# Performance work log

Measured on AMD Instinct MI355X. Metric: run time of the kernel, lower is better.

## Reference

```python
import jax, jax.numpy as jnp
import numpy as np

N = 50000          # nodes
E = 625000         # edges
H = 128            # hidden_dim
L = 4              # num_layers
G = 2000           # number of graphs in batch
NODE_F = 9
EDGE_F = 4
LN_EPS = 1e-5


def setup_inputs() -> dict:
    key = jax.random.key(0)
    ks = jax.random.split(key, 14)
    s = 0.05
    return {
        "x": jax.random.normal(ks[0], (N, NODE_F), jnp.float32),
        "edge_index": jax.random.randint(ks[1], (2, E), 0, N, dtype=jnp.int32),
        "edge_attr": jax.random.normal(ks[2], (E, EDGE_F), jnp.float32),
        "batch": jnp.sort(jax.random.randint(ks[3], (N,), 0, G, dtype=jnp.int32)),
        # node / edge encoders
        "Wn": jax.random.normal(ks[4], (NODE_F, H), jnp.float32) * s,
        "bn": jnp.zeros((H,), jnp.float32),
        "We": jax.random.normal(ks[5], (EDGE_F, H), jnp.float32) * s,
        "be": jnp.zeros((H,), jnp.float32),
        # per-layer GINE MLP params (stacked over layers)
        "W1": jax.random.normal(ks[6], (L, H, 2 * H), jnp.float32) * s,
        "b1": jnp.zeros((L, 2 * H), jnp.float32),
        "W2": jax.random.normal(ks[7], (L, 2 * H, H), jnp.float32) * s,
        "b2": jnp.zeros((L, H), jnp.float32),
        # per-layer LayerNorm params
        "gamma": jnp.ones((L, H), jnp.float32),
        "beta": jnp.zeros((L, H), jnp.float32),
    }


def reference(x, edge_index, edge_attr, batch, Wn, bn, We, be, W1, b1, W2, b2, gamma, beta):
    h = x @ Wn + bn                       # [N, H]
    ea = edge_attr @ We + be              # [E, H]
    src, dst = edge_index[0], edge_index[1]
    for l in range(L):
        res = h
        # GINEConv (eps=0): out = mlp(x + sum_j relu(x_j + e_ij))
        msg = jax.nn.relu(h[src] + ea)                              # [E, H] gather+add+relu
        agg = jax.ops.segment_sum(msg, dst, num_segments=N)        # scatter-sum -> [N, H]
        z = h + agg
        z = jax.nn.relu(z @ W1[l] + b1[l]) @ W2[l] + b2[l]          # 2-layer MLP
        mu = jnp.mean(z, axis=-1, keepdims=True)
        var = jnp.mean((z - mu) ** 2, axis=-1, keepdims=True)
        z = (z - mu) * jax.lax.rsqrt(var + LN_EPS) * gamma[l] + beta[l]
        h = jax.nn.relu(z) + res                                    # relu + residual
    # global_add_pool
    return jax.ops.segment_sum(h, batch, num_segments=G)            # [G, H]
```

## Files before the change

### kernel.cpp

```cpp
#include <hip/hip_runtime.h>

typedef unsigned short ushort_t;
typedef __attribute__((ext_vector_type(8))) __bf16 bf16x8;
typedef __attribute__((ext_vector_type(4))) float f32x4;

#define HD 128
#define NL 4
#define SCAN_C 2048

__device__ __forceinline__ ushort_t f2bf(float f){
  unsigned u = __builtin_bit_cast(unsigned, f);
  unsigned r = (u + 0x7FFFu + ((u >> 16) & 1u)) >> 16;
  return (ushort_t)r;
}

__device__ __forceinline__ float bf2f(ushort_t u){
  unsigned v = ((unsigned)u) << 16;
  return __builtin_bit_cast(float, v);
}

__device__ __forceinline__ f32x4 mfma16(bf16x8 a, bf16x8 b, f32x4 c){
  return __builtin_amdgcn_mfma_f32_16x16x32_bf16(a, b, c, 0, 0, 0);
}

__global__ void hist_kernel(const int* __restrict__ dst, int* __restrict__ deg, int E){
  int e = blockIdx.x * 256 + threadIdx.x;
  if (e < E) atomicAdd(&deg[dst[e]], 1);
}

__global__ void gbound_kernel(const int* __restrict__ batch, int* __restrict__ goff,
                              int N, int G){
  int n = blockIdx.x * 256 + threadIdx.x;
  if (n >= N) return;
  int bc = batch[n];
  int bp = (n == 0) ? -1 : batch[n - 1];
  for (int g = bp + 1; g <= bc; ++g) goff[g] = n;
  if (n == N - 1)
    for (int g = bc + 1; g <= G; ++g) goff[g] = N;
}

__global__ void scan_part(const int* __restrict__ in, int* __restrict__ bsum, int n){
  int b = blockIdx.x, tid = threadIdx.x;
  int base = b * SCAN_C + tid * 8;
  int s = 0;
  if (base + 8 <= n){
    int4 a = *(const int4*)(in + base);
    int4 c = *(const int4*)(in + base + 4);
    s = a.x + a.y + a.z + a.w + c.x + c.y + c.z + c.w;
  } else {
    #pragma unroll
    for (int k = 0; k < 8; ++k) if (base + k < n) s += in[base + k];
  }
  #pragma unroll
  for (int o = 1; o < 64; o <<= 1) s += __shfl_xor(s, o, 64);
  __shared__ int ws[4];
  int lane = tid & 63, wid = tid >> 6;
  if (lane == 0) ws[wid] = s;
  __syncthreads();
  if (tid == 0) bsum[b] = ws[0] + ws[1] + ws[2] + ws[3];
}

__global__ void scan_top(const int* __restrict__ bsum, int* __restrict__ bofs,
                         int* __restrict__ outn, int B){
  int tid = threadIdx.x;
  int v = (tid < B) ? bsum[tid] : 0;
  int lane = tid & 63, wid = tid >> 6;
  int inc = v;
  #pragma unroll
  for (int o = 1; o < 64; o <<= 1){
    int t = __shfl_up(inc, o, 64);
    if (lane >= o) inc += t;
  }
  __shared__ int ws[4];
  if (lane == 63) ws[wid] = inc;
  __syncthreads();
  int wprev = 0;
  for (int i = 0; i < wid; ++i) wprev += ws[i];
  if (tid < B) bofs[tid] = inc - v + wprev;
  if (tid == 0) *outn = ws[0] + ws[1] + ws[2] + ws[3];
}

__global__ void scan_final(const int* __restrict__ in, const int* __restrict__ bofs,
                           int* __restrict__ out, int* __restrict__ cur, int n){
  int b = blockIdx.x, tid = threadIdx.x;
  int base = b * SCAN_C + tid * 8;
  int v[8];
  if (base + 8 <= n){
    *(int4*)(v)     = *(const int4*)(in + base);
    *(int4*)(v + 4) = *(const int4*)(in + base + 4);
  } else {
    #pragma unroll
    for (int k = 0; k < 8; ++k) v[k] = (base + k < n) ? in[base + k] : 0;
  }
  int tsum = 0;
  #pragma unroll
  for (int k = 0; k < 8; ++k) tsum += v[k];
  int lane = tid & 63, wid = tid >> 6;
  int inc = tsum;
  #pragma unroll
  for (int o = 1; o < 64; o <<= 1){
    int t = __shfl_up(inc, o, 64);
    if (lane >= o) inc += t;
  }
  __shared__ int ws[4];
  if (lane == 63) ws[wid] = inc;
  __syncthreads();
  int run = bofs[b] + inc - tsum;
  for (int i = 0; i < wid; ++i) run += ws[i];
  #pragma unroll
  for (int k = 0; k < 8; ++k){
    int i = base + k;
    if (i < n){
      out[i] = run;
      if (cur) cur[i] = run;
      run += v[k];
    }
  }
}

__global__ void scatter_kernel(const int* __restrict__ dst, int* __restrict__ cursor,
                               int* __restrict__ perm, int E){
  int e = blockIdx.x * 256 + threadIdx.x;
  if (e < E){
    int d = dst[e];
    int p = atomicAdd(&cursor[d], 1);
    perm[p] = e;
  }
}

__global__ void permute_kernel(const int* __restrict__ perm, const int* __restrict__ src,
                               const float4* __restrict__ ea, int* __restrict__ srcs_s,
                               float4* __restrict__ ea4p, int E){
  int p = blockIdx.x * 256 + threadIdx.x;
  if (p < E){
    int e = perm[p];
    srcs_s[p] = src[e];
    ea4p[p] = ea[e];
  }
}

__global__ void wconv_kernel(const float* __restrict__ W1, const float* __restrict__ W2,
                             ushort_t* __restrict__ W1t, ushort_t* __restrict__ W2t){
  int i = blockIdx.x * 256 + threadIdx.x;
  if (i < NL * 32768){
    int l = i >> 15, r = i & 32767;
    int n = r >> 7, k = r & 127;
    W1t[i] = f2bf(W1[l * 32768 + k * 256 + n]);
  } else {
    int i2 = i - NL * 32768;
    int l = i2 >> 15, r = i2 & 32767;
    int n = r >> 8, k = r & 255;
    W2t[i2] = f2bf(W2[l * 32768 + k * 128 + n]);
  }
}

__global__ void encoder_kernel(const float* __restrict__ x, const float* __restrict__ Wn,
                               const float* __restrict__ bn, float* __restrict__ h,
                               ushort_t* __restrict__ hb, int N){
  int n = blockIdx.x, j = threadIdx.x;
  float acc = bn[j];
  #pragma unroll
  for (int k = 0; k < 9; ++k) acc = fmaf(x[n * 9 + k], Wn[k * HD + j], acc);
  h[(size_t)n * HD + j] = acc;
  hb[(size_t)n * HD + j] = f2bf(acc);
}

__global__ void agg_kernel(const float* __restrict__ h, const ushort_t* __restrict__ hb,
                           const int* __restrict__ off, const int* __restrict__ srcs,
                           const float4* __restrict__ ea4, const float* __restrict__ We,
                           const float* __restrict__ be, ushort_t* __restrict__ z, int N){
  int n = blockIdx.x, j = threadIdx.x;
  float w0 = We[j], w1 = We[HD + j], w2 = We[2 * HD + j], w3 = We[3 * HD + j];
  float bj = be[j];
  int s = off[n], e = off[n + 1];
  float acc = h[(size_t)n * HD + j];
  int i = s;
  for (; i + 8 <= e; i += 8){
    int s0 = srcs[i],     s1 = srcs[i + 1], s2 = srcs[i + 2], s3 = srcs[i + 3];
    int s4 = srcs[i + 4], s5 = srcs[i + 5], s6 = srcs[i + 6], s7 = srcs[i + 7];
    ushort_t g0 = hb[(size_t)s0 * HD + j];
    ushort_t g1 = hb[(size_t)s1 * HD + j];
    ushort_t g2 = hb[(size_t)s2 * HD + j];
    ushort_t g3 = hb[(size_t)s3 * HD + j];
    ushort_t g4 = hb[(size_t)s4 * HD + j];
    ushort_t g5 = hb[(size_t)s5 * HD + j];
    ushort_t g6 = hb[(size_t)s6 * HD + j];
    ushort_t g7 = hb[(size_t)s7 * HD + j];
    {
      float4 a0 = ea4[i], a1 = ea4[i + 1], a2 = ea4[i + 2], a3 = ea4[i + 3];
      float e0 = fmaf(a0.x, w0, fmaf(a0.y, w1, fmaf(a0.z, w2, fmaf(a0.w, w3, bj))));
      float e1 = fmaf(a1.x, w0, fmaf(a1.y, w1, fmaf(a1.z, w2, fmaf(a1.w, w3, bj))));
      float e2 = fmaf(a2.x, w0, fmaf(a2.y, w1, fmaf(a2.z, w2, fmaf(a2.w, w3, bj))));
      float e3 = fmaf(a3.x, w0, fmaf(a3.y, w1, fmaf(a3.z, w2, fmaf(a3.w, w3, bj))));
      acc += fmaxf(bf2f(g0) + e0, 0.f);
      acc += fmaxf(bf2f(g1) + e1, 0.f);
      acc += fmaxf(bf2f(g2) + e2, 0.f);
      acc += fmaxf(bf2f(g3) + e3, 0.f);
    }
    {
      float4 a4 = ea4[i + 4], a5 = ea4[i + 5], a6 = ea4[i + 6], a7 = ea4[i + 7];
      float e4 = fmaf(a4.x, w0, fmaf(a4.y, w1, fmaf(a4.z, w2, fmaf(a4.w, w3, bj))));
      float e5 = fmaf(a5.x, w0, fmaf(a5.y, w1, fmaf(a5.z, w2, fmaf(a5.w, w3, bj))));
      float e6 = fmaf(a6.x, w0, fmaf(a6.y, w1, fmaf(a6.z, w2, fmaf(a6.w, w3, bj))));
      float e7 = fmaf(a7.x, w0, fmaf(a7.y, w1, fmaf(a7.z, w2, fmaf(a7.w, w3, bj))));
      acc += fmaxf(bf2f(g4) + e4, 0.f);
      acc += fmaxf(bf2f(g5) + e5, 0.f);
      acc += fmaxf(bf2f(g6) + e6, 0.f);
      acc += fmaxf(bf2f(g7) + e7, 0.f);
    }
  }
  for (; i + 4 <= e; i += 4){
    int s0 = srcs[i], s1 = srcs[i + 1], s2 = srcs[i + 2], s3 = srcs[i + 3];
    float4 a0 = ea4[i], a1 = ea4[i + 1], a2 = ea4[i + 2], a3 = ea4[i + 3];
    float h0 = bf2f(hb[(size_t)s0 * HD + j]);
    float h1 = bf2f(hb[(size_t)s1 * HD + j]);
    float h2 = bf2f(hb[(size_t)s2 * HD + j]);
    float h3 = bf2f(hb[(size_t)s3 * HD + j]);
    float e0 = fmaf(a0.x, w0, fmaf(a0.y, w1, fmaf(a0.z, w2, fmaf(a0.w, w3, bj))));
    float e1 = fmaf(a1.x, w0, fmaf(a1.y, w1, fmaf(a1.z, w2, fmaf(a1.w, w3, bj))));
    float e2 = fmaf(a2.x, w0, fmaf(a2.y, w1, fmaf(a2.z, w2, fmaf(a2.w, w3, bj))));
    float e3 = fmaf(a3.x, w0, fmaf(a3.y, w1, fmaf(a3.z, w2, fmaf(a3.w, w3, bj))));
    acc += fmaxf(h0 + e0, 0.f);
    acc += fmaxf(h1 + e1, 0.f);
    acc += fmaxf(h2 + e2, 0.f);
    acc += fmaxf(h3 + e3, 0.f);
  }
  for (; i < e; ++i){
    int sc = srcs[i];
    float4 a = ea4[i];
    float eav = fmaf(a.x, w0, fmaf(a.y, w1, fmaf(a.z, w2, fmaf(a.w, w3, bj))));
    acc += fmaxf(bf2f(hb[(size_t)sc * HD + j]) + eav, 0.f);
  }
  z[(size_t)n * HD + j] = f2bf(acc);
}

__global__ __launch_bounds__(512, 4) void mlp_fused_kernel(
    const ushort_t* __restrict__ zin, const ushort_t* __restrict__ W1t,
    const float* __restrict__ b1, const ushort_t* __restrict__ W2t,
    const float* __restrict__ b2, const float* __restrict__ gamma,
    const float* __restrict__ beta, float* __restrict__ h,
    ushort_t* __restrict__ hb, int N){
  extern __shared__ char lds[];
  int tid = threadIdx.x;
  int r0 = blockIdx.x * 128;
  #pragma unroll
  for (int i = 0; i < 4; ++i){
    int g = i * 512 + tid;
    int row = g >> 4, kg = g & 15;
    int lb = row * 256 + ((kg * 16) ^ ((row & 7) << 4));
    int ar = min(r0 + row, N - 1);
    *(bf16x8*)(lds + lb) = *(const bf16x8*)(zin + (size_t)ar * 128 + kg * 8);
  }
  int w = tid >> 6, l = tid & 63;
  int lr = l & 15, lk = l >> 4;
  int wk = w >> 1, wn = w & 1;
  bf16x8 aN[4];
  #pragma unroll
  for (int fm = 0; fm < 4; ++fm)
    aN[fm] = *(const bf16x8*)((const char*)W1t +
              (size_t)(wk * 64 + fm * 16 + lr) * 256 + lk * 16);
  __syncthreads();
  {
    f32x4 acc1[4][4] = {};
    #pragma unroll
    for (int ks = 0; ks < 4; ++ks){
      int kb = ks * 64 + lk * 16;
      bf16x8 aC[4];
      #pragma unroll
      for (int fm = 0; fm < 4; ++fm) aC[fm] = aN[fm];
      if (ks < 3){
        int kbn = (ks + 1) * 64 + lk * 16;
        #pragma unroll
        for (int fm = 0; fm < 4; ++fm)
          aN[fm] = *(const bf16x8*)((const char*)W1t +
                    (size_t)(wk * 64 + fm * 16 + lr) * 256 + kbn);
      }
      bf16x8 b[4];
      #pragma unroll
      for (int fn = 0; fn < 4; ++fn){
        int node = wn * 64 + fn * 16 + lr;
        b[fn] = *(const bf16x8*)(lds + node * 256 + (kb ^ ((node & 7) << 4)));
      }
      #pragma unroll
      for (int fm = 0; fm < 4; ++fm)
        #pragma unroll
        for (int fn = 0; fn < 4; ++fn)
          acc1[fm][fn] = mfma16(aC[fm], b[fn], acc1[fm][fn]);
    }
    __syncthreads();
    #pragma unroll
    for (int fm = 0; fm < 4; ++fm){
      f32x4 bv = *(const f32x4*)(b1 + wk * 64 + fm * 16 + lk * 4);
      int k2b = (wk * 64 + fm * 16 + lk * 4) * 2;
      #pragma unroll
      for (int fn = 0; fn < 4; ++fn){
        int node = wn * 64 + fn * 16 + lr;
        ushort4 tv;
        tv.x = f2bf(fmaxf(acc1[fm][fn][0] + bv[0], 0.f));
        tv.y = f2bf(fmaxf(acc1[fm][fn][1] + bv[1], 0.f));
        tv.z = f2bf(fmaxf(acc1[fm][fn][2] + bv[2], 0.f));
        tv.w = f2bf(fmaxf(acc1[fm][fn][3] + bv[3], 0.f));
        *(ushort4*)(lds + node * 512 + (k2b ^ ((node & 7) << 4))) = tv;
      }
    }
  }
  int wd = w >> 1, wn2 = w & 1;
  bf16x8 a2N[2];
  #pragma unroll
  for (int fm = 0; fm < 2; ++fm)
    a2N[fm] = *(const bf16x8*)((const char*)W2t +
               (size_t)(wd * 32 + fm * 16 + lr) * 512 + lk * 16);
  __syncthreads();
  f32x4 acc2[2][4] = {};
  #pragma unroll
  for (int ks = 0; ks < 8; ++ks){
    int kb = ks * 64 + lk * 16;
    bf16x8 a2C[2];
    #pragma unroll
    for (int fm = 0; fm < 2; ++fm) a2C[fm] = a2N[fm];
    if (ks < 7){
      int kbn = (ks + 1) * 64 + lk * 16;
      #pragma unroll
      for (int fm = 0; fm < 2; ++fm)
        a2N[fm] = *(const bf16x8*)((const char*)W2t +
                   (size_t)(wd * 32 + fm * 16 + lr) * 512 + kbn);
    }
    bf16x8 bt2[4];
    #pragma unroll
    for (int fn = 0; fn < 4; ++fn){
      int node = wn2 * 64 + fn * 16 + lr;
      bt2[fn] = *(const bf16x8*)(lds + node * 512 + (kb ^ ((node & 7) << 4)));
    }
    #pragma unroll
    for (int fm = 0; fm < 2; ++fm)
      #pragma unroll
      for (int fn = 0; fn < 4; ++fn)
        acc2[fm][fn] = mfma16(a2C[fm], bt2[fn], acc2[fm][fn]);
  }
  __syncthreads();
  float* stat_s = (float*)lds;
  float* stat_q = (float*)(lds + 2048);
  f32x4 b2v[2], gv[2], btv[2];
  #pragma unroll
  for (int fm = 0; fm < 2; ++fm){
    int db = wd * 32 + fm * 16 + lk * 4;
    b2v[fm] = *(const f32x4*)(b2 + db);
    gv[fm]  = *(const f32x4*)(gamma + db);
    btv[fm] = *(const f32x4*)(beta + db);
  }
  #pragma unroll
  for (int fn = 0; fn < 4; ++fn){
    float ss = 0.f, qq = 0.f;
    #pragma unroll
    for (int fm = 0; fm < 2; ++fm)
      #pragma unroll
      for (int r = 0; r < 4; ++r){
        float v = acc2[fm][fn][r] + b2v[fm][r];
        acc2[fm][fn][r] = v;
        ss += v; qq += v * v;
      }
    ss += __shfl_xor(ss, 16, 64); ss += __shfl_xor(ss, 32, 64);
    qq += __shfl_xor(qq, 16, 64); qq += __shfl_xor(qq, 32, 64);
    if (l < 16){
      int node = wn2 * 64 + fn * 16 + lr;
      stat_s[node * 4 + wd] = ss;
      stat_q[node * 4 + wd] = qq;
    }
  }
  __syncthreads();
  #pragma unroll
  for (int fn = 0; fn < 4; ++fn){
    int node = wn2 * 64 + fn * 16 + lr;
    int gn = r0 + node;
    float ss = stat_s[node * 4 + 0] + stat_s[node * 4 + 1] +
               stat_s[node * 4 + 2] + stat_s[node * 4 + 3];
    float qq = stat_q[node * 4 + 0] + stat_q[node * 4 + 1] +
               stat_q[node * 4 + 2] + stat_q[node * 4 + 3];
    float mean = ss * (1.f / 128.f);
    float rs = rsqrtf(qq * (1.f / 128.f) - mean * mean + 1e-5f);
    if (gn < N){
      #pragma unroll
      for (int fm = 0; fm < 2; ++fm){
        int db = wd * 32 + fm * 16 + lk * 4;
        f32x4 hold = *(const f32x4*)(h + (size_t)gn * HD + db);
        f32x4 ov;
        #pragma unroll
        for (int r = 0; r < 4; ++r)
          ov[r] = fmaxf((acc2[fm][fn][r] - mean) * rs * gv[fm][r] + btv[fm][r], 0.f) + hold[r];
        *(f32x4*)(h + (size_t)gn * HD + db) = ov;
        ushort4 hv;
        hv.x = f2bf(ov[0]); hv.y = f2bf(ov[1]); hv.z = f2bf(ov[2]); hv.w = f2bf(ov[3]);
        *(ushort4*)(hb + (size_t)gn * HD + db) = hv;
      }
    }
  }
}

__global__ void pool_kernel(const float* __restrict__ h, const int* __restrict__ goff,
                            float* __restrict__ outp, int G){
  int g = blockIdx.x, j = threadIdx.x;
  int s = goff[g], e = goff[g + 1];
  float acc = 0.f;
  for (int i = s; i < e; ++i) acc += h[(size_t)i * HD + j];
  outp[(size_t)g * HD + j] = acc;
}

extern "C" void kernel_launch(void* const* d_in, const int* in_sizes, int n_in,
                              void* d_out, int out_size, void* d_ws, size_t ws_size,
                              hipStream_t stream){
  const float* x     = (const float*)d_in[0];
  const int*   ei    = (const int*)  d_in[1];
  const float* eattr = (const float*)d_in[2];
  const int*   batch = (const int*)  d_in[3];
  const float* Wn    = (const float*)d_in[4];
  const float* bn    = (const float*)d_in[5];
  const float* We    = (const float*)d_in[6];
  const float* be    = (const float*)d_in[7];
  const float* W1    = (const float*)d_in[8];
  const float* b1    = (const float*)d_in[9];
  const float* W2    = (const float*)d_in[10];
  const float* b2    = (const float*)d_in[11];
  const float* gamma = (const float*)d_in[12];
  const float* beta  = (const float*)d_in[13];
  float* outp = (float*)d_out;

  int N = in_sizes[3];
  int E = in_sizes[2] / 4;
  int G = out_size / HD;

  char* base = (char*)d_ws;
  size_t o = 0;
  auto alloc = [&](size_t bytes)->char*{
    char* r = base + o; o = (o + bytes + 255) & ~(size_t)255; return r;
  };
  float*    h    = (float*)   alloc((size_t)N * HD * 4);
  ushort_t* hb   = (ushort_t*)alloc((size_t)N * HD * 2);
  ushort_t* z    = (ushort_t*)alloc((size_t)N * HD * 2);
  ushort_t* W1t  = (ushort_t*)alloc((size_t)NL * 2 * HD * HD * 2);
  ushort_t* W2t  = (ushort_t*)alloc((size_t)NL * 2 * HD * HD * 2);
  int* deg    = (int*)alloc((size_t)N * 4);
  int* off    = (int*)alloc((size_t)(N + 1) * 4);
  int* goff   = (int*)alloc((size_t)(G + 1) * 4);
  int* cursor = (int*)alloc((size_t)N * 4);
  int* bsumN  = (int*)alloc(512 * 4);
  int* bofsN  = (int*)alloc(512 * 4);
  int* perm   = (int*)alloc((size_t)E * 4);
  int* srcs_s = (int*)alloc((size_t)E * 4);
  float4* ea4p= (float4*)alloc((size_t)E * 16);
  (void)ws_size; (void)n_in;

  const int* src = ei;
  const int* dst = ei + E;

  hipMemsetAsync(deg, 0, (size_t)N * 4, stream);

  hist_kernel<<<(E + 255) / 256, 256, 0, stream>>>(dst, deg, E);
  gbound_kernel<<<(N + 255) / 256, 256, 0, stream>>>(batch, goff, N, G);

  int BN = (N + SCAN_C - 1) / SCAN_C;
  scan_part<<<BN, 256, 0, stream>>>(deg, bsumN, N);
  scan_top<<<1, 256, 0, stream>>>(bsumN, bofsN, off + N, BN);
  scan_final<<<BN, 256, 0, stream>>>(deg, bofsN, off, cursor, N);

  scatter_kernel<<<(E + 255) / 256, 256, 0, stream>>>(dst, cursor, perm, E);
  permute_kernel<<<(E + 255) / 256, 256, 0, stream>>>(perm, src, (const float4*)eattr,
                                                      srcs_s, ea4p, E);
  wconv_kernel<<<(2 * NL * 32768) / 256, 256, 0, stream>>>(W1, W2, W1t, W2t);
  encoder_kernel<<<N, HD, 0, stream>>>(x, Wn, bn, h, hb, N);

  int mblocks = (N + 127) / 128;
  for (int l = 0; l < NL; ++l){
    agg_kernel<<<N, HD, 0, stream>>>(h, hb, off, srcs_s, ea4p, We, be, z, N);
    mlp_fused_kernel<<<mblocks, 512, 65536, stream>>>(
        z, W1t + (size_t)l * 2 * HD * HD, b1 + l * 2 * HD,
        W2t + (size_t)l * 2 * HD * HD, b2 + l * HD,
        gamma + l * HD, beta + l * HD, h, hb, N);
  }
  pool_kernel<<<G, HD, 0, stream>>>(h, goff, outp, G);
}
```

Baseline: 404.0 us.

## Fuse neighbor aggregation into the MLP layer kernel with ping-pong bf16 buffers

```diff
diff --git a/kernel.cpp b/kernel.cpp
--- a/kernel.cpp
+++ b/kernel.cpp
@@ -165,91 +165,90 @@
   hb[(size_t)n * HD + j] = f2bf(acc);
 }
 
-__global__ void agg_kernel(const float* __restrict__ h, const ushort_t* __restrict__ hb,
-                           const int* __restrict__ off, const int* __restrict__ srcs,
-                           const float4* __restrict__ ea4, const float* __restrict__ We,
-                           const float* __restrict__ be, ushort_t* __restrict__ z, int N){
-  int n = blockIdx.x, j = threadIdx.x;
-  float w0 = We[j], w1 = We[HD + j], w2 = We[2 * HD + j], w3 = We[3 * HD + j];
-  float bj = be[j];
-  int s = off[n], e = off[n + 1];
-  float acc = h[(size_t)n * HD + j];
-  int i = s;
-  for (; i + 8 <= e; i += 8){
-    int s0 = srcs[i],     s1 = srcs[i + 1], s2 = srcs[i + 2], s3 = srcs[i + 3];
-    int s4 = srcs[i + 4], s5 = srcs[i + 5], s6 = srcs[i + 6], s7 = srcs[i + 7];
-    ushort_t g0 = hb[(size_t)s0 * HD + j];
-    ushort_t g1 = hb[(size_t)s1 * HD + j];
-    ushort_t g2 = hb[(size_t)s2 * HD + j];
-    ushort_t g3 = hb[(size_t)s3 * HD + j];
-    ushort_t g4 = hb[(size_t)s4 * HD + j];
-    ushort_t g5 = hb[(size_t)s5 * HD + j];
-    ushort_t g6 = hb[(size_t)s6 * HD + j];
-    ushort_t g7 = hb[(size_t)s7 * HD + j];
-    {
-      float4 a0 = ea4[i], a1 = ea4[i + 1], a2 = ea4[i + 2], a3 = ea4[i + 3];
-      float e0 = fmaf(a0.x, w0, fmaf(a0.y, w1, fmaf(a0.z, w2, fmaf(a0.w, w3, bj))));
-      float e1 = fmaf(a1.x, w0, fmaf(a1.y, w1, fmaf(a1.z, w2, fmaf(a1.w, w3, bj))));
-      float e2 = fmaf(a2.x, w0, fmaf(a2.y, w1, fmaf(a2.z, w2, fmaf(a2.w, w3, bj))));
-      float e3 = fmaf(a3.x, w0, fmaf(a3.y, w1, fmaf(a3.z, w2, fmaf(a3.w, w3, bj))));
-      acc += fmaxf(bf2f(g0) + e0, 0.f);
-      acc += fmaxf(bf2f(g1) + e1, 0.f);
-      acc += fmaxf(bf2f(g2) + e2, 0.f);
-      acc += fmaxf(bf2f(g3) + e3, 0.f);
-    }
-    {
-      float4 a4 = ea4[i + 4], a5 = ea4[i + 5], a6 = ea4[i + 6], a7 = ea4[i + 7];
-      float e4 = fmaf(a4.x, w0, fmaf(a4.y, w1, fmaf(a4.z, w2, fmaf(a4.w, w3, bj))));
-      float e5 = fmaf(a5.x, w0, fmaf(a5.y, w1, fmaf(a5.z, w2, fmaf(a5.w, w3, bj))));
-      float e6 = fmaf(a6.x, w0, fmaf(a6.y, w1, fmaf(a6.z, w2, fmaf(a6.w, w3, bj))));
-      float e7 = fmaf(a7.x, w0, fmaf(a7.y, w1, fmaf(a7.z, w2, fmaf(a7.w, w3, bj))));
-      acc += fmaxf(bf2f(g4) + e4, 0.f);
-      acc += fmaxf(bf2f(g5) + e5, 0.f);
-      acc += fmaxf(bf2f(g6) + e6, 0.f);
-      acc += fmaxf(bf2f(g7) + e7, 0.f);
-    }
-  }
-  for (; i + 4 <= e; i += 4){
-    int s0 = srcs[i], s1 = srcs[i + 1], s2 = srcs[i + 2], s3 = srcs[i + 3];
-    float4 a0 = ea4[i], a1 = ea4[i + 1], a2 = ea4[i + 2], a3 = ea4[i + 3];
-    float h0 = bf2f(hb[(size_t)s0 * HD + j]);
-    float h1 = bf2f(hb[(size_t)s1 * HD + j]);
-    float h2 = bf2f(hb[(size_t)s2 * HD + j]);
-    float h3 = bf2f(hb[(size_t)s3 * HD + j]);
-    float e0 = fmaf(a0.x, w0, fmaf(a0.y, w1, fmaf(a0.z, w2, fmaf(a0.w, w3, bj))));
-    float e1 = fmaf(a1.x, w0, fmaf(a1.y, w1, fmaf(a1.z, w2, fmaf(a1.w, w3, bj))));
-    float e2 = fmaf(a2.x, w0, fmaf(a2.y, w1, fmaf(a2.z, w2, fmaf(a2.w, w3, bj))));
-    float e3 = fmaf(a3.x, w0, fmaf(a3.y, w1, fmaf(a3.z, w2, fmaf(a3.w, w3, bj))));
-    acc += fmaxf(h0 + e0, 0.f);
-    acc += fmaxf(h1 + e1, 0.f);
-    acc += fmaxf(h2 + e2, 0.f);
-    acc += fmaxf(h3 + e3, 0.f);
-  }
-  for (; i < e; ++i){
-    int sc = srcs[i];
-    float4 a = ea4[i];
-    float eav = fmaf(a.x, w0, fmaf(a.y, w1, fmaf(a.z, w2, fmaf(a.w, w3, bj))));
-    acc += fmaxf(bf2f(hb[(size_t)sc * HD + j]) + eav, 0.f);
-  }
-  z[(size_t)n * HD + j] = f2bf(acc);
-}
-
-__global__ __launch_bounds__(512, 4) void mlp_fused_kernel(
-    const ushort_t* __restrict__ zin, const ushort_t* __restrict__ W1t,
-    const float* __restrict__ b1, const ushort_t* __restrict__ W2t,
-    const float* __restrict__ b2, const float* __restrict__ gamma,
-    const float* __restrict__ beta, float* __restrict__ h,
-    ushort_t* __restrict__ hb, int N){
+__global__ __launch_bounds__(512, 4) void layer_kernel(
+    float* __restrict__ h, const ushort_t* __restrict__ hbi,
+    ushort_t* __restrict__ hbo, const int* __restrict__ off,
+    const int* __restrict__ srcs, const float4* __restrict__ ea4,
+    const float* __restrict__ We, const float* __restrict__ be,
+    const ushort_t* __restrict__ W1t, const float* __restrict__ b1,
+    const ushort_t* __restrict__ W2t, const float* __restrict__ b2,
+    const float* __restrict__ gamma, const float* __restrict__ beta, int N){
   extern __shared__ char lds[];
   int tid = threadIdx.x;
   int r0 = blockIdx.x * 128;
-  #pragma unroll
-  for (int i = 0; i < 4; ++i){
-    int g = i * 512 + tid;
-    int row = g >> 4, kg = g & 15;
-    int lb = row * 256 + ((kg * 16) ^ ((row & 7) << 4));
-    int ar = min(r0 + row, N - 1);
-    *(bf16x8*)(lds + lb) = *(const bf16x8*)(zin + (size_t)ar * 128 + kg * 8);
+  {
+    int j = tid & 127;
+    int q = tid >> 7;
+    float w0 = We[j], w1 = We[HD + j], w2 = We[2 * HD + j], w3 = We[3 * HD + j];
+    float bj = be[j];
+    for (int c = 0; c < 32; ++c){
+      int nl = q * 32 + c;
+      int node = r0 + nl;
+      float acc = 0.f;
+      if (node < N){
+        int s = off[node], e = off[node + 1];
+        acc = h[(size_t)node * HD + j];
+        int i = s;
+        for (; i + 8 <= e; i += 8){
+          int s0 = srcs[i],     s1 = srcs[i + 1], s2 = srcs[i + 2], s3 = srcs[i + 3];
+          int s4 = srcs[i + 4], s5 = srcs[i + 5], s6 = srcs[i + 6], s7 = srcs[i + 7];
+          ushort_t g0 = hbi[(size_t)s0 * HD + j];
+          ushort_t g1 = hbi[(size_t)s1 * HD + j];
+          ushort_t g2 = hbi[(size_t)s2 * HD + j];
+          ushort_t g3 = hbi[(size_t)s3 * HD + j];
+          ushort_t g4 = hbi[(size_t)s4 * HD + j];
+          ushort_t g5 = hbi[(size_t)s5 * HD + j];
+          ushort_t g6 = hbi[(size_t)s6 * HD + j];
+          ushort_t g7 = hbi[(size_t)s7 * HD + j];
+          {
+            float4 a0 = ea4[i], a1 = ea4[i + 1], a2 = ea4[i + 2], a3 = ea4[i + 3];
+            float e0 = fmaf(a0.x, w0, fmaf(a0.y, w1, fmaf(a0.z, w2, fmaf(a0.w, w3, bj))));
+            float e1 = fmaf(a1.x, w0, fmaf(a1.y, w1, fmaf(a1.z, w2, fmaf(a1.w, w3, bj))));
+            float e2 = fmaf(a2.x, w0, fmaf(a2.y, w1, fmaf(a2.z, w2, fmaf(a2.w, w3, bj))));
+            float e3 = fmaf(a3.x, w0, fmaf(a3.y, w1, fmaf(a3.z, w2, fmaf(a3.w, w3, bj))));
+            acc += fmaxf(bf2f(g0) + e0, 0.f);
+            acc += fmaxf(bf2f(g1) + e1, 0.f);
+            acc += fmaxf(bf2f(g2) + e2, 0.f);
+            acc += fmaxf(bf2f(g3) + e3, 0.f);
+          }
+          {
+            float4 a4 = ea4[i + 4], a5 = ea4[i + 5], a6 = ea4[i + 6], a7 = ea4[i + 7];
+            float e4 = fmaf(a4.x, w0, fmaf(a4.y, w1, fmaf(a4.z, w2, fmaf(a4.w, w3, bj))));
+            float e5 = fmaf(a5.x, w0, fmaf(a5.y, w1, fmaf(a5.z, w2, fmaf(a5.w, w3, bj))));
+            float e6 = fmaf(a6.x, w0, fmaf(a6.y, w1, fmaf(a6.z, w2, fmaf(a6.w, w3, bj))));
+            float e7 = fmaf(a7.x, w0, fmaf(a7.y, w1, fmaf(a7.z, w2, fmaf(a7.w, w3, bj))));
+            acc += fmaxf(bf2f(g4) + e4, 0.f);
+            acc += fmaxf(bf2f(g5) + e5, 0.f);
+            acc += fmaxf(bf2f(g6) + e6, 0.f);
+            acc += fmaxf(bf2f(g7) + e7, 0.f);
+          }
+        }
+        for (; i + 4 <= e; i += 4){
+          int s0 = srcs[i], s1 = srcs[i + 1], s2 = srcs[i + 2], s3 = srcs[i + 3];
+          float4 a0 = ea4[i], a1 = ea4[i + 1], a2 = ea4[i + 2], a3 = ea4[i + 3];
+          float h0 = bf2f(hbi[(size_t)s0 * HD + j]);
+          float h1 = bf2f(hbi[(size_t)s1 * HD + j]);
+          float h2 = bf2f(hbi[(size_t)s2 * HD + j]);
+          float h3 = bf2f(hbi[(size_t)s3 * HD + j]);
+          float e0 = fmaf(a0.x, w0, fmaf(a0.y, w1, fmaf(a0.z, w2, fmaf(a0.w, w3, bj))));
+          float e1 = fmaf(a1.x, w0, fmaf(a1.y, w1, fmaf(a1.z, w2, fmaf(a1.w, w3, bj))));
+          float e2 = fmaf(a2.x, w0, fmaf(a2.y, w1, fmaf(a2.z, w2, fmaf(a2.w, w3, bj))));
+          float e3 = fmaf(a3.x, w0, fmaf(a3.y, w1, fmaf(a3.z, w2, fmaf(a3.w, w3, bj))));
+          acc += fmaxf(h0 + e0, 0.f);
+          acc += fmaxf(h1 + e1, 0.f);
+          acc += fmaxf(h2 + e2, 0.f);
+          acc += fmaxf(h3 + e3, 0.f);
+        }
+        for (; i < e; ++i){
+          int sc = srcs[i];
+          float4 a = ea4[i];
+          float eav = fmaf(a.x, w0, fmaf(a.y, w1, fmaf(a.z, w2, fmaf(a.w, w3, bj))));
+          acc += fmaxf(bf2f(hbi[(size_t)sc * HD + j]) + eav, 0.f);
+        }
+      }
+      int boff = (2 * j) ^ ((nl & 7) << 4);
+      *(ushort_t*)(lds + nl * 256 + boff) = f2bf(acc);
+    }
   }
   int w = tid >> 6, l = tid & 63;
   int lr = l & 15, lk = l >> 4;
@@ -390,7 +389,7 @@
         *(f32x4*)(h + (size_t)gn * HD + db) = ov;
         ushort4 hv;
         hv.x = f2bf(ov[0]); hv.y = f2bf(ov[1]); hv.z = f2bf(ov[2]); hv.w = f2bf(ov[3]);
-        *(ushort4*)(hb + (size_t)gn * HD + db) = hv;
+        *(ushort4*)(hbo + (size_t)gn * HD + db) = hv;
       }
     }
   }
@@ -434,8 +433,8 @@
     char* r = base + o; o = (o + bytes + 255) & ~(size_t)255; return r;
   };
   float*    h    = (float*)   alloc((size_t)N * HD * 4);
-  ushort_t* hb   = (ushort_t*)alloc((size_t)N * HD * 2);
-  ushort_t* z    = (ushort_t*)alloc((size_t)N * HD * 2);
+  ushort_t* hb0  = (ushort_t*)alloc((size_t)N * HD * 2);
+  ushort_t* hb1  = (ushort_t*)alloc((size_t)N * HD * 2);
   ushort_t* W1t  = (ushort_t*)alloc((size_t)NL * 2 * HD * HD * 2);
   ushort_t* W2t  = (ushort_t*)alloc((size_t)NL * 2 * HD * HD * 2);
   int* deg    = (int*)alloc((size_t)N * 4);
@@ -466,15 +465,18 @@
   permute_kernel<<<(E + 255) / 256, 256, 0, stream>>>(perm, src, (const float4*)eattr,
                                                       srcs_s, ea4p, E);
   wconv_kernel<<<(2 * NL * 32768) / 256, 256, 0, stream>>>(W1, W2, W1t, W2t);
-  encoder_kernel<<<N, HD, 0, stream>>>(x, Wn, bn, h, hb, N);
+  encoder_kernel<<<N, HD, 0, stream>>>(x, Wn, bn, h, hb0, N);
 
   int mblocks = (N + 127) / 128;
+  ushort_t* hbin = hb0;
+  ushort_t* hbout = hb1;
   for (int l = 0; l < NL; ++l){
-    agg_kernel<<<N, HD, 0, stream>>>(h, hb, off, srcs_s, ea4p, We, be, z, N);
-    mlp_fused_kernel<<<mblocks, 512, 65536, stream>>>(
-        z, W1t + (size_t)l * 2 * HD * HD, b1 + l * 2 * HD,
+    layer_kernel<<<mblocks, 512, 65536, stream>>>(
+        h, hbin, hbout, off, srcs_s, ea4p, We, be,
+        W1t + (size_t)l * 2 * HD * HD, b1 + l * 2 * HD,
         W2t + (size_t)l * 2 * HD * HD, b2 + l * HD,
-        gamma + l * HD, beta + l * HD, h, hb, N);
+        gamma + l * HD, beta + l * HD, N);
+    ushort_t* tmp = hbin; hbin = hbout; hbout = tmp;
   }
   pool_kernel<<<G, HD, 0, stream>>>(h, goff, outp, G);
 }
```

After: 622.6 us. +54.1%, slower.
